# Optimization experiments

Hardware: AMD Instinct MI355X
Metric: run time of the kernel (lower is better)

## Reference

```python
import math
import jax, jax.numpy as jnp
import numpy as np

L = 2          # num_layers
B = 2          # micro batch
S = 2048       # seq_length
H = 1024       # hidden_size
NH = 16        # num_attention_heads
DH = 64        # kv_channels (head dim)
FF = 4096      # ffn_hidden_size
EPS = 1e-5
STD = 0.0048


def setup_inputs() -> dict:
    key = jax.random.key(0)
    ks = jax.random.split(key, 12)
    out_std = STD / math.sqrt(2.0 * L)
    # ALiBi slopes for NH=16 (power of 2)
    start = 2.0 ** (-2.0 ** (-(math.log2(NH) - 3)))
    slopes = np.array([start * start ** i for i in range(NH)], dtype=np.float32)
    alibi = slopes[None, :, None, None] * np.arange(S, dtype=np.float32)[None, None, None, :]
    alibi = jnp.asarray(np.broadcast_to(alibi, (B, NH, 1, S)))  # [B, NH, 1, S]
    return {
        "hidden_states": jax.random.normal(ks[0], (B, S, H), jnp.float32),
        "alibi": alibi,
        "qkv_w": jax.random.normal(ks[1], (L, 3 * NH * DH, H), jnp.float32) * STD,
        "qkv_b": jnp.zeros((L, 3 * NH * DH), jnp.float32),
        "dense_w": jax.random.normal(ks[2], (L, H, NH * DH), jnp.float32) * out_std,
        "dense_b": jnp.zeros((L, H), jnp.float32),
        "mlp_w1": jax.random.normal(ks[3], (L, FF, H), jnp.float32) * STD,
        "mlp_b1": jnp.zeros((L, FF), jnp.float32),
        "mlp_w2": jax.random.normal(ks[4], (L, H, FF), jnp.float32) * out_std,
        "mlp_b2": jnp.zeros((L, H), jnp.float32),
        "ln1_w": jnp.ones((L, H), jnp.float32),
        "ln1_b": jnp.zeros((L, H), jnp.float32),
        "ln2_w": jnp.ones((L, H), jnp.float32),
        "ln2_b": jnp.zeros((L, H), jnp.float32),
    }


def _layernorm(x, w, b):
    mu = jnp.mean(x, axis=-1, keepdims=True)
    var = jnp.mean(jnp.square(x - mu), axis=-1, keepdims=True)
    return (x - mu) * jax.lax.rsqrt(var + EPS) * w + b


def _layer(x, alibi, causal, layer_number, qkv_w, qkv_b, dense_w, dense_b,
           mlp_w1, mlp_b1, mlp_w2, mlp_b2, ln1_w, ln1_b, ln2_w, ln2_b):
    # --- attention ---
    h = _layernorm(x, ln1_w, ln1_b)
    qkv = h @ qkv_w.T + qkv_b                       # [B, S, 3*NH*DH]
    q, k, v = jnp.split(qkv, 3, axis=-1)
    q = q.reshape(B, S, NH, DH).transpose(0, 2, 1, 3)  # [B, NH, S, DH]
    k = k.reshape(B, S, NH, DH).transpose(0, 2, 1, 3)
    v = v.reshape(B, S, NH, DH).transpose(0, 2, 1, 3)
    norm_factor = math.sqrt(DH) * layer_number
    beta = 1.0 / layer_number
    alpha = 1.0 / norm_factor
    scores = beta * alibi + alpha * jnp.einsum("bhqd,bhkd->bhqk", q, k)
    # ScaleMaskSoftmax: scale by layer_number, causal mask fill -10000, softmax
    scores = scores * layer_number
    scores = jnp.where(causal, scores, jnp.float32(-10000.0))
    probs = jax.nn.softmax(scores, axis=-1)
    ctx = jnp.einsum("bhqk,bhkd->bhqd", probs, v)   # [B, NH, S, DH]
    ctx = ctx.transpose(0, 2, 1, 3).reshape(B, S, NH * DH)
    attn_out = ctx @ dense_w.T + dense_b
    x = x + attn_out
    # --- MLP ---
    h2 = _layernorm(x, ln2_w, ln2_b)
    m = jax.nn.gelu(h2 @ mlp_w1.T + mlp_b1, approximate=False)
    m = m @ mlp_w2.T + mlp_b2
    return x + m


def reference(hidden_states, alibi, qkv_w, qkv_b, dense_w, dense_b,
              mlp_w1, mlp_b1, mlp_w2, mlp_b2, ln1_w, ln1_b, ln2_w, ln2_b):
    causal = jnp.tril(jnp.ones((S, S), dtype=bool))[None, None]  # [1,1,S,S]
    x = hidden_states
    for l in range(L):
        x = _layer(x, alibi, causal, l + 1,
                   qkv_w[l], qkv_b[l], dense_w[l], dense_b[l],
                   mlp_w1[l], mlp_b1[l], mlp_w2[l], mlp_b2[l],
                   ln1_w[l], ln1_b[l], ln2_w[l], ln2_b[l])
    return x
```

## Files before the change

kernel.cpp:

```cpp
#include <hip/hip_runtime.h>
#include <cstdint>
#include <cmath>

#define SS 2048
#define HH 1024

typedef __bf16 bf16_t;
typedef __bf16 bf16x8 __attribute__((ext_vector_type(8)));
typedef __bf16 bf16x4 __attribute__((ext_vector_type(4)));
typedef float  f32x4  __attribute__((ext_vector_type(4)));

union U32P { unsigned u; bf16_t h[2]; };

__device__ __forceinline__ void async_load16(const void* g, void* l) {
  __builtin_amdgcn_global_load_lds(
      (__attribute__((address_space(1))) void*)(g),
      (__attribute__((address_space(3))) void*)(l), 16, 0, 0);
}

__global__ __launch_bounds__(256) void cvt_kernel(const float* __restrict__ in,
                                                  bf16_t* __restrict__ out) {
  size_t i = (size_t)blockIdx.x * 256 + threadIdx.x;
  f32x4 v = ((const f32x4*)in)[i];
  bf16x4 o;
  o[0] = (bf16_t)v[0]; o[1] = (bf16_t)v[1]; o[2] = (bf16_t)v[2]; o[3] = (bf16_t)v[3];
  ((bf16x4*)out)[i] = o;
}

__global__ __launch_bounds__(256) void ln_kernel(const float* __restrict__ x,
                                                 const float* __restrict__ w,
                                                 const float* __restrict__ b,
                                                 bf16_t* __restrict__ out) {
  const int row = blockIdx.x;
  const int tid = threadIdx.x;
  const f32x4 v = ((const f32x4*)(x + (size_t)row * HH))[tid];
  float s  = v[0] + v[1] + v[2] + v[3];
  float s2 = v[0]*v[0] + v[1]*v[1] + v[2]*v[2] + v[3]*v[3];
#pragma unroll
  for (int o = 1; o < 64; o <<= 1) { s += __shfl_xor(s, o); s2 += __shfl_xor(s2, o); }
  __shared__ float r1[4], r2[4];
  if ((tid & 63) == 0) { r1[tid >> 6] = s; r2[tid >> 6] = s2; }
  __syncthreads();
  float ts  = r1[0] + r1[1] + r1[2] + r1[3];
  float ts2 = r2[0] + r2[1] + r2[2] + r2[3];
  float mu  = ts * (1.0f / HH);
  float var = ts2 * (1.0f / HH) - mu * mu;
  float rstd = rsqrtf(var + 1e-5f);
  f32x4 wv = ((const f32x4*)w)[tid];
  f32x4 bv = ((const f32x4*)b)[tid];
  bf16x4 o;
#pragma unroll
  for (int j = 0; j < 4; ++j) o[j] = (bf16_t)((v[j] - mu) * rstd * wv[j] + bv[j]);
  ((bf16x4*)(out + (size_t)row * HH))[tid] = o;
}

__device__ __forceinline__ float gelu_f(float x) {
  return 0.5f * x * (1.0f + erff(x * 0.70710678118654752f));
}

__global__ __launch_bounds__(256) void fuse_add(float* __restrict__ x,
                                                const bf16_t* __restrict__ p0,
                                                const bf16_t* __restrict__ p1,
                                                const float* __restrict__ bias) {
  size_t i = (size_t)blockIdx.x * 256 + threadIdx.x;
  f32x4 xv = ((f32x4*)x)[i];
  bf16x4 a = ((const bf16x4*)p0)[i];
  bf16x4 b4 = ((const bf16x4*)p1)[i];
  f32x4 bv = ((const f32x4*)bias)[i & 255];
#pragma unroll
  for (int j = 0; j < 4; ++j) xv[j] += (float)a[j] + (float)b4[j] + bv[j];
  ((f32x4*)x)[i] = xv;
}

template <int EPI>
__global__ __launch_bounds__(256) void gemm_bt(const bf16_t* __restrict__ A,
                                               const bf16_t* __restrict__ W,
                                               const float* __restrict__ bias,
                                               bf16_t* __restrict__ outb,
                                               int M, int N, int K) {
  __shared__ __align__(16) bf16_t As[128 * 64];
  __shared__ __align__(16) bf16_t Bs[128 * 64];
  const int tid = threadIdx.x;
  const int w = tid >> 6, lane = tid & 63;
  const int m16 = lane & 15, quad = lane >> 4;
  const int wm = w & 1, wn = w >> 1;
  const int n0 = blockIdx.x * 128, m0 = blockIdx.y * 128;

  f32x4 acc[4][4];
#pragma unroll
  for (int i = 0; i < 4; ++i)
#pragma unroll
    for (int j = 0; j < 4; ++j) acc[i][j] = (f32x4){0.f, 0.f, 0.f, 0.f};

  int rowi[4], gci[4];
#pragma unroll
  for (int i = 0; i < 4; ++i) {
    int p = (w * 4 + i) * 64 + lane;
    rowi[i] = p >> 3;
    gci[i] = ((lane & 7) ^ (rowi[i] & 7)) * 8;
  }

  for (int kt = 0; kt < K; kt += 64) {
    __syncthreads();
#pragma unroll
    for (int i = 0; i < 4; ++i) {
      async_load16(A + (size_t)(m0 + rowi[i]) * K + kt + gci[i], &As[(w * 4 + i) * 512]);
      async_load16(W + (size_t)(n0 + rowi[i]) * K + kt + gci[i], &Bs[(w * 4 + i) * 512]);
    }
    __syncthreads();
#pragma unroll
    for (int kk = 0; kk < 2; ++kk) {
      bf16x8 af[4], bfv[4];
#pragma unroll
      for (int mi = 0; mi < 4; ++mi) {
        int row = wm * 64 + mi * 16 + m16;
        int cpos = (kk * 4 + quad) ^ (row & 7);
        af[mi] = *(const bf16x8*)&As[row * 64 + cpos * 8];
      }
#pragma unroll
      for (int ni = 0; ni < 4; ++ni) {
        int row = wn * 64 + ni * 16 + m16;
        int cpos = (kk * 4 + quad) ^ (row & 7);
        bfv[ni] = *(const bf16x8*)&Bs[row * 64 + cpos * 8];
      }
#pragma unroll
      for (int mi = 0; mi < 4; ++mi)
#pragma unroll
        for (int ni = 0; ni < 4; ++ni)
          acc[mi][ni] = __builtin_amdgcn_mfma_f32_16x16x32_bf16(af[mi], bfv[ni],
                                                                acc[mi][ni], 0, 0, 0);
    }
  }

#pragma unroll
  for (int ni = 0; ni < 4; ++ni) {
    int col = n0 + wn * 64 + ni * 16 + m16;
    float bv = bias[col];
#pragma unroll
    for (int mi = 0; mi < 4; ++mi) {
      int rowb = m0 + wm * 64 + mi * 16 + quad * 4;
#pragma unroll
      for (int r = 0; r < 4; ++r) {
        size_t idx = (size_t)(rowb + r) * N + col;
        float v = acc[mi][ni][r] + bv;
        if constexpr (EPI == 1) v = gelu_f(v);
        outb[idx] = (bf16_t)v;
      }
    }
  }
}

__global__ __launch_bounds__(256) void gemm_sk2(const bf16_t* __restrict__ A,
                                                const bf16_t* __restrict__ W,
                                                bf16_t* __restrict__ p0,
                                                bf16_t* __restrict__ p1,
                                                int M, int N, int K) {
  __shared__ __align__(16) bf16_t As[128 * 64];
  __shared__ __align__(16) bf16_t Bs[128 * 64];
  const int tid = threadIdx.x;
  const int w = tid >> 6, lane = tid & 63;
  const int m16 = lane & 15, quad = lane >> 4;
  const int wm = w & 1, wn = w >> 1;
  const int n0 = blockIdx.x * 128, m0 = blockIdx.y * 128;
  const int z = blockIdx.z;
  const int kbeg = z * (K >> 1), kend = kbeg + (K >> 1);
  bf16_t* outb = z ? p1 : p0;

  f32x4 acc[4][4];
#pragma unroll
  for (int i = 0; i < 4; ++i)
#pragma unroll
    for (int j = 0; j < 4; ++j) acc[i][j] = (f32x4){0.f, 0.f, 0.f, 0.f};

  int rowi[4], gci[4];
#pragma unroll
  for (int i = 0; i < 4; ++i) {
    int p = (w * 4 + i) * 64 + lane;
    rowi[i] = p >> 3;
    gci[i] = ((lane & 7) ^ (rowi[i] & 7)) * 8;
  }

  for (int kt = kbeg; kt < kend; kt += 64) {
    __syncthreads();
#pragma unroll
    for (int i = 0; i < 4; ++i) {
      async_load16(A + (size_t)(m0 + rowi[i]) * K + kt + gci[i], &As[(w * 4 + i) * 512]);
      async_load16(W + (size_t)(n0 + rowi[i]) * K + kt + gci[i], &Bs[(w * 4 + i) * 512]);
    }
    __syncthreads();
#pragma unroll
    for (int kk = 0; kk < 2; ++kk) {
      bf16x8 af[4], bfv[4];
#pragma unroll
      for (int mi = 0; mi < 4; ++mi) {
        int row = wm * 64 + mi * 16 + m16;
        int cpos = (kk * 4 + quad) ^ (row & 7);
        af[mi] = *(const bf16x8*)&As[row * 64 + cpos * 8];
      }
#pragma unroll
      for (int ni = 0; ni < 4; ++ni) {
        int row = wn * 64 + ni * 16 + m16;
        int cpos = (kk * 4 + quad) ^ (row & 7);
        bfv[ni] = *(const bf16x8*)&Bs[row * 64 + cpos * 8];
      }
#pragma unroll
      for (int mi = 0; mi < 4; ++mi)
#pragma unroll
        for (int ni = 0; ni < 4; ++ni)
          acc[mi][ni] = __builtin_amdgcn_mfma_f32_16x16x32_bf16(af[mi], bfv[ni],
                                                                acc[mi][ni], 0, 0, 0);
    }
  }

#pragma unroll
  for (int ni = 0; ni < 4; ++ni) {
    int col = n0 + wn * 64 + ni * 16 + m16;
#pragma unroll
    for (int mi = 0; mi < 4; ++mi) {
      int rowb = m0 + wm * 64 + mi * 16 + quad * 4;
#pragma unroll
      for (int r = 0; r < 4; ++r) {
        size_t idx = (size_t)(rowb + r) * N + col;
        outb[idx] = (bf16_t)acc[mi][ni][r];
      }
    }
  }
}

__global__ __launch_bounds__(256) void attn_kernel(const bf16_t* __restrict__ qkv,
                                                   bf16_t* __restrict__ ctx) {
  const int qt = 31 - blockIdx.y;
  const int bh = blockIdx.x;
  const int b = bh >> 4, h = bh & 15;
  const int tid = threadIdx.x;
  const int w = tid >> 6, lane = tid & 63;
  const int m16 = lane & 15, quad = lane >> 4;

  __shared__ __align__(16) bf16_t Vt[2][64 * 72];
  __shared__ __align__(16) bf16_t Pl[4][16 * 72];

  const float slope2 = __builtin_amdgcn_exp2f(-0.70710678118654752f * (float)(h + 1))
                       * 1.4426950408889634f;
  const int wt = (int)((30.0f / slope2 + 63.0f) * 0.015625f);
  const int kt0 = (qt - wt > 0) ? (qt - wt) : 0;

  const int q_abs = qt * 64 + w * 16 + m16;
  float alkb[16];
#pragma unroll
  for (int kn = 0; kn < 4; ++kn)
#pragma unroll
    for (int r = 0; r < 4; ++r)
      alkb[kn * 4 + r] = slope2 * (float)(kt0 * 64 + kn * 16 + quad * 4 + r - q_abs);
  const float d64 = slope2 * 64.0f;

  const int qrow = qt * 64 + w * 16 + m16;
  const bf16_t* qbase = qkv + (size_t)(b * SS + qrow) * 3072 + h * 64;
  const bf16x8 bq0 = *(const bf16x8*)(qbase + quad * 8);
  const bf16x8 bq1 = *(const bf16x8*)(qbase + 32 + quad * 8);

  const bf16_t* kbase = qkv + (size_t)(b * SS + m16) * 3072 + 1024 + h * 64 + quad * 8;
  const int kp2 = (tid & 31) * 2, vd0 = (tid >> 5) * 8;
  const bf16_t* vsrc = qkv + (size_t)(b * SS + kp2) * 3072 + 2048 + h * 64 + vd0;
  const int ql = w * 16 + m16;
  constexpr float C = 0.18033688011112042f;

  f32x4 acc[4];
#pragma unroll
  for (int i = 0; i < 4; ++i) acc[i] = (f32x4){0.f, 0.f, 0.f, 0.f};
  float rs_l = 0.f;

  bf16x8 ak[4][2], v0, v1;
  {
    const bf16_t* kb = kbase + (size_t)kt0 * 64 * 3072;
#pragma unroll
    for (int kn = 0; kn < 4; ++kn) {
      ak[kn][0] = *(const bf16x8*)(kb + (size_t)(kn * 16) * 3072);
      ak[kn][1] = *(const bf16x8*)(kb + (size_t)(kn * 16) * 3072 + 32);
    }
    const bf16_t* vs = vsrc + (size_t)kt0 * 64 * 3072;
    v0 = *(const bf16x8*)(vs);
    v1 = *(const bf16x8*)(vs + 3072);
  }
#pragma unroll
  for (int j = 0; j < 8; ++j) {
    U32P pk; pk.h[0] = v0[j]; pk.h[1] = v1[j];
    *(unsigned*)&Vt[kt0 & 1][(vd0 + j) * 72 + kp2] = pk.u;
  }

  for (int kt = kt0; kt <= qt; ++kt) {
    __syncthreads();

    bf16x8 nk[4][2], nv0 = v0, nv1 = v1;
    if (kt < qt) {
      const bf16_t* kb = kbase + (size_t)(kt + 1) * 64 * 3072;
#pragma unroll
      for (int kn = 0; kn < 4; ++kn) {
        nk[kn][0] = *(const bf16x8*)(kb + (size_t)(kn * 16) * 3072);
        nk[kn][1] = *(const bf16x8*)(kb + (size_t)(kn * 16) * 3072 + 32);
      }
      const bf16_t* nsrc = vsrc + (size_t)(kt + 1) * 64 * 3072;
      nv0 = *(const bf16x8*)(nsrc);
      nv1 = *(const bf16x8*)(nsrc + 3072);
    } else {
#pragma unroll
      for (int kn = 0; kn < 4; ++kn) { nk[kn][0] = ak[kn][0]; nk[kn][1] = ak[kn][1]; }
    }

    float p[16];
    const bool diag = (kt == qt);
#pragma unroll
    for (int kn = 0; kn < 4; ++kn) {
      f32x4 z = (f32x4){0.f, 0.f, 0.f, 0.f};
      z = __builtin_amdgcn_mfma_f32_16x16x32_bf16(ak[kn][0], bq0, z, 0, 0, 0);
      z = __builtin_amdgcn_mfma_f32_16x16x32_bf16(ak[kn][1], bq1, z, 0, 0, 0);
#pragma unroll
      for (int r = 0; r < 4; ++r) {
        float s = fmaf(z[r], C, alkb[kn * 4 + r]);
        if (diag) {
          int kl = kn * 16 + quad * 4 + r;
          if (kl > ql) s = -INFINITY;
        }
        float e = __builtin_amdgcn_exp2f(s);
        p[kn * 4 + r] = e;
        rs_l += e;
      }
    }
#pragma unroll
    for (int i = 0; i < 16; ++i) alkb[i] += d64;

#pragma unroll
    for (int kn = 0; kn < 4; ++kn) {
      U32P a, c;
      a.h[0] = (bf16_t)p[kn * 4 + 0]; a.h[1] = (bf16_t)p[kn * 4 + 1];
      c.h[0] = (bf16_t)p[kn * 4 + 2]; c.h[1] = (bf16_t)p[kn * 4 + 3];
      uint2 pk; pk.x = a.u; pk.y = c.u;
      *(uint2*)&Pl[w][m16 * 72 + kn * 16 + quad * 4] = pk;
    }
    const bf16_t* vt = &Vt[kt & 1][0];
    bf16x8 bp0 = *(const bf16x8*)&Pl[w][m16 * 72 + quad * 8];
    bf16x8 bp1 = *(const bf16x8*)&Pl[w][m16 * 72 + 32 + quad * 8];
#pragma unroll
    for (int ni = 0; ni < 4; ++ni) {
      bf16x8 av0 = *(const bf16x8*)&vt[(ni * 16 + m16) * 72 + quad * 8];
      bf16x8 av1 = *(const bf16x8*)&vt[(ni * 16 + m16) * 72 + 32 + quad * 8];
      acc[ni] = __builtin_amdgcn_mfma_f32_16x16x32_bf16(av0, bp0, acc[ni], 0, 0, 0);
      acc[ni] = __builtin_amdgcn_mfma_f32_16x16x32_bf16(av1, bp1, acc[ni], 0, 0, 0);
    }

    if (kt < qt) {
#pragma unroll
      for (int j = 0; j < 8; ++j) {
        U32P pk; pk.h[0] = nv0[j]; pk.h[1] = nv1[j];
        *(unsigned*)&Vt[(kt + 1) & 1][(vd0 + j) * 72 + kp2] = pk.u;
      }
    }
#pragma unroll
    for (int kn = 0; kn < 4; ++kn) { ak[kn][0] = nk[kn][0]; ak[kn][1] = nk[kn][1]; }
    v0 = nv0; v1 = nv1;
  }

  rs_l += __shfl_xor(rs_l, 16);
  rs_l += __shfl_xor(rs_l, 32);
  const float inv_l = 1.0f / rs_l;
  bf16_t* cb = ctx + (size_t)(b * SS + qt * 64 + w * 16 + m16) * 1024 + h * 64;
#pragma unroll
  for (int ni = 0; ni < 4; ++ni) {
    U32P a, c;
    a.h[0] = (bf16_t)(acc[ni][0] * inv_l); a.h[1] = (bf16_t)(acc[ni][1] * inv_l);
    c.h[0] = (bf16_t)(acc[ni][2] * inv_l); c.h[1] = (bf16_t)(acc[ni][3] * inv_l);
    uint2 pk; pk.x = a.u; pk.y = c.u;
    *(uint2*)(cb + ni * 16 + quad * 4) = pk;
  }
}

extern "C" void kernel_launch(void* const* d_in, const int* in_sizes, int n_in,
                              void* d_out, int out_size, void* d_ws, size_t ws_size,
                              hipStream_t stream) {
  const float* hs    = (const float*)d_in[0];
  const float* qkvw  = (const float*)d_in[2];
  const float* qkvb  = (const float*)d_in[3];
  const float* dw    = (const float*)d_in[4];
  const float* db    = (const float*)d_in[5];
  const float* w1    = (const float*)d_in[6];
  const float* b1    = (const float*)d_in[7];
  const float* w2    = (const float*)d_in[8];
  const float* b2    = (const float*)d_in[9];
  const float* ln1w  = (const float*)d_in[10];
  const float* ln1b  = (const float*)d_in[11];
  const float* ln2w  = (const float*)d_in[12];
  const float* ln2b  = (const float*)d_in[13];
  float* x = (float*)d_out;

  char* ws = (char*)d_ws;
  bf16_t* wqc = (bf16_t*)(ws + 0);
  bf16_t* wdc = (bf16_t*)(ws + 12582912);
  bf16_t* w1c = (bf16_t*)(ws + 16777216);
  bf16_t* w2c = (bf16_t*)(ws + 33554432);
  bf16_t* hb  = (bf16_t*)(ws + 50331648);
  bf16_t* qm  = (bf16_t*)(ws + 58720256);
  bf16_t* cx  = (bf16_t*)(ws + 92274688);
  bf16_t* dp0 = qm;
  bf16_t* dp1 = qm + (size_t)4096 * 1024;

  hipMemcpyAsync(x, hs, (size_t)4096 * 1024 * 4, hipMemcpyDeviceToDevice, stream);
  cvt_kernel<<<6144, 256, 0, stream>>>(qkvw, wqc);
  cvt_kernel<<<2048, 256, 0, stream>>>(dw, wdc);
  cvt_kernel<<<8192, 256, 0, stream>>>(w1, w1c);
  cvt_kernel<<<8192, 256, 0, stream>>>(w2, w2c);

  for (int l = 0; l < 2; ++l) {
    ln_kernel<<<4096, 256, 0, stream>>>(x, ln1w + l * 1024, ln1b + l * 1024, hb);
    gemm_bt<0><<<dim3(24, 32), 256, 0, stream>>>(hb, wqc + (size_t)l * 3145728,
        qkvb + l * 3072, qm, 4096, 3072, 1024);
    attn_kernel<<<dim3(32, 32), 256, 0, stream>>>(qm, cx);
    gemm_sk2<<<dim3(8, 32, 2), 256, 0, stream>>>(cx, wdc + (size_t)l * 1048576,
        dp0, dp1, 4096, 1024, 1024);
    fuse_add<<<4096, 256, 0, stream>>>(x, dp0, dp1, db + l * 1024);
    ln_kernel<<<4096, 256, 0, stream>>>(x, ln2w + l * 1024, ln2b + l * 1024, hb);
    gemm_bt<1><<<dim3(32, 32), 256, 0, stream>>>(hb, w1c + (size_t)l * 4194304,
        b1 + l * 4096, qm, 4096, 4096, 1024);
    gemm_sk2<<<dim3(8, 32, 2), 256, 0, stream>>>(qm, w2c + (size_t)l * 4194304,
        hb, cx, 4096, 1024, 4096);
    fuse_add<<<4096, 256, 0, stream>>>(x, hb, cx, b2 + l * 1024);
  }
}
```

Before: 705.7 us.

## Double-buffer GEMM shared-memory tiles and fuse residual add with layernorm

Both bf16 GEMM kernels now keep two LDS tiles per operand. The next K-tile is prefetched with async global-to-LDS loads while the current one is fed to MFMA, which cuts the two barriers per iteration down to one and overlaps load latency with compute. Separately, the residual add of the split-K partial sums is fused with the following layernorm in a new fuse_add_ln kernel, so x is not re-read in a separate LN pass. The doubled LDS footprint (64 KB per block) may lower the number of blocks resident per CU.

```diff
diff --git a/kernel.cpp b/kernel.cpp
--- a/kernel.cpp
+++ b/kernel.cpp
@@ -72,14 +72,51 @@
   ((f32x4*)x)[i] = xv;
 }
 
+__global__ __launch_bounds__(256) void fuse_add_ln(float* __restrict__ x,
+                                                   const bf16_t* __restrict__ p0,
+                                                   const bf16_t* __restrict__ p1,
+                                                   const float* __restrict__ bias,
+                                                   const float* __restrict__ lw,
+                                                   const float* __restrict__ lb,
+                                                   bf16_t* __restrict__ out) {
+  const int row = blockIdx.x;
+  const int tid = threadIdx.x;
+  const size_t i = (size_t)row * 256 + tid;
+  f32x4 xv = ((f32x4*)x)[i];
+  bf16x4 a = ((const bf16x4*)p0)[i];
+  bf16x4 b4 = ((const bf16x4*)p1)[i];
+  f32x4 bv = ((const f32x4*)bias)[tid];
+#pragma unroll
+  for (int j = 0; j < 4; ++j) xv[j] += (float)a[j] + (float)b4[j] + bv[j];
+  ((f32x4*)x)[i] = xv;
+  float s  = xv[0] + xv[1] + xv[2] + xv[3];
+  float s2 = xv[0]*xv[0] + xv[1]*xv[1] + xv[2]*xv[2] + xv[3]*xv[3];
+#pragma unroll
+  for (int o = 1; o < 64; o <<= 1) { s += __shfl_xor(s, o); s2 += __shfl_xor(s2, o); }
+  __shared__ float r1[4], r2[4];
+  if ((tid & 63) == 0) { r1[tid >> 6] = s; r2[tid >> 6] = s2; }
+  __syncthreads();
+  float ts  = r1[0] + r1[1] + r1[2] + r1[3];
+  float ts2 = r2[0] + r2[1] + r2[2] + r2[3];
+  float mu  = ts * (1.0f / HH);
+  float var = ts2 * (1.0f / HH) - mu * mu;
+  float rstd = rsqrtf(var + 1e-5f);
+  f32x4 wv  = ((const f32x4*)lw)[tid];
+  f32x4 lbv = ((const f32x4*)lb)[tid];
+  bf16x4 o;
+#pragma unroll
+  for (int j = 0; j < 4; ++j) o[j] = (bf16_t)((xv[j] - mu) * rstd * wv[j] + lbv[j]);
+  ((bf16x4*)(out + (size_t)row * HH))[tid] = o;
+}
+
 template <int EPI>
 __global__ __launch_bounds__(256) void gemm_bt(const bf16_t* __restrict__ A,
                                                const bf16_t* __restrict__ W,
                                                const float* __restrict__ bias,
                                                bf16_t* __restrict__ outb,
                                                int M, int N, int K) {
-  __shared__ __align__(16) bf16_t As[128 * 64];
-  __shared__ __align__(16) bf16_t Bs[128 * 64];
+  __shared__ __align__(16) bf16_t As[2][128 * 64];
+  __shared__ __align__(16) bf16_t Bs[2][128 * 64];
   const int tid = threadIdx.x;
   const int w = tid >> 6, lane = tid & 63;
   const int m16 = lane & 15, quad = lane >> 4;
@@ -100,14 +137,26 @@
     gci[i] = ((lane & 7) ^ (rowi[i] & 7)) * 8;
   }
 
-  for (int kt = 0; kt < K; kt += 64) {
+#pragma unroll
+  for (int i = 0; i < 4; ++i) {
+    async_load16(A + (size_t)(m0 + rowi[i]) * K + gci[i], &As[0][(w * 4 + i) * 512]);
+    async_load16(W + (size_t)(n0 + rowi[i]) * K + gci[i], &Bs[0][(w * 4 + i) * 512]);
+  }
+
+  const int NT = K >> 6;
+  for (int t = 0; t < NT; ++t) {
+    const int cur = t & 1;
     __syncthreads();
-#pragma unroll
-    for (int i = 0; i < 4; ++i) {
-      async_load16(A + (size_t)(m0 + rowi[i]) * K + kt + gci[i], &As[(w * 4 + i) * 512]);
-      async_load16(W + (size_t)(n0 + rowi[i]) * K + kt + gci[i], &Bs[(w * 4 + i) * 512]);
-    }
-    __syncthreads();
+    if (t + 1 < NT) {
+      const int kt = (t + 1) << 6;
+#pragma unroll
+      for (int i = 0; i < 4; ++i) {
+        async_load16(A + (size_t)(m0 + rowi[i]) * K + kt + gci[i],
+                     &As[cur ^ 1][(w * 4 + i) * 512]);
+        async_load16(W + (size_t)(n0 + rowi[i]) * K + kt + gci[i],
+                     &Bs[cur ^ 1][(w * 4 + i) * 512]);
+      }
+    }
 #pragma unroll
     for (int kk = 0; kk < 2; ++kk) {
       bf16x8 af[4], bfv[4];
@@ -115,13 +164,13 @@
       for (int mi = 0; mi < 4; ++mi) {
         int row = wm * 64 + mi * 16 + m16;
         int cpos = (kk * 4 + quad) ^ (row & 7);
-        af[mi] = *(const bf16x8*)&As[row * 64 + cpos * 8];
+        af[mi] = *(const bf16x8*)&As[cur][row * 64 + cpos * 8];
       }
 #pragma unroll
       for (int ni = 0; ni < 4; ++ni) {
         int row = wn * 64 + ni * 16 + m16;
         int cpos = (kk * 4 + quad) ^ (row & 7);
-        bfv[ni] = *(const bf16x8*)&Bs[row * 64 + cpos * 8];
+        bfv[ni] = *(const bf16x8*)&Bs[cur][row * 64 + cpos * 8];
       }
 #pragma unroll
       for (int mi = 0; mi < 4; ++mi)
@@ -155,15 +204,15 @@
                                                 bf16_t* __restrict__ p0,
                                                 bf16_t* __restrict__ p1,
                                                 int M, int N, int K) {
-  __shared__ __align__(16) bf16_t As[128 * 64];
-  __shared__ __align__(16) bf16_t Bs[128 * 64];
+  __shared__ __align__(16) bf16_t As[2][128 * 64];
+  __shared__ __align__(16) bf16_t Bs[2][128 * 64];
   const int tid = threadIdx.x;
   const int w = tid >> 6, lane = tid & 63;
   const int m16 = lane & 15, quad = lane >> 4;
   const int wm = w & 1, wn = w >> 1;
   const int n0 = blockIdx.x * 128, m0 = blockIdx.y * 128;
   const int z = blockIdx.z;
-  const int kbeg = z * (K >> 1), kend = kbeg + (K >> 1);
+  const int kbeg = z * (K >> 1);
   bf16_t* outb = z ? p1 : p0;
 
   f32x4 acc[4][4];
@@ -180,14 +229,26 @@
     gci[i] = ((lane & 7) ^ (rowi[i] & 7)) * 8;
   }
 
-  for (int kt = kbeg; kt < kend; kt += 64) {
+#pragma unroll
+  for (int i = 0; i < 4; ++i) {
+    async_load16(A + (size_t)(m0 + rowi[i]) * K + kbeg + gci[i], &As[0][(w * 4 + i) * 512]);
+    async_load16(W + (size_t)(n0 + rowi[i]) * K + kbeg + gci[i], &Bs[0][(w * 4 + i) * 512]);
+  }
+
+  const int NT = K >> 7;
+  for (int t = 0; t < NT; ++t) {
+    const int cur = t & 1;
     __syncthreads();
-#pragma unroll
-    for (int i = 0; i < 4; ++i) {
-      async_load16(A + (size_t)(m0 + rowi[i]) * K + kt + gci[i], &As[(w * 4 + i) * 512]);
-      async_load16(W + (size_t)(n0 + rowi[i]) * K + kt + gci[i], &Bs[(w * 4 + i) * 512]);
-    }
-    __syncthreads();
+    if (t + 1 < NT) {
+      const int kt = kbeg + ((t + 1) << 6);
+#pragma unroll
+      for (int i = 0; i < 4; ++i) {
+        async_load16(A + (size_t)(m0 + rowi[i]) * K + kt + gci[i],
+                     &As[cur ^ 1][(w * 4 + i) * 512]);
+        async_load16(W + (size_t)(n0 + rowi[i]) * K + kt + gci[i],
+                     &Bs[cur ^ 1][(w * 4 + i) * 512]);
+      }
+    }
 #pragma unroll
     for (int kk = 0; kk < 2; ++kk) {
       bf16x8 af[4], bfv[4];
@@ -195,13 +256,13 @@
       for (int mi = 0; mi < 4; ++mi) {
         int row = wm * 64 + mi * 16 + m16;
         int cpos = (kk * 4 + quad) ^ (row & 7);
-        af[mi] = *(const bf16x8*)&As[row * 64 + cpos * 8];
+        af[mi] = *(const bf16x8*)&As[cur][row * 64 + cpos * 8];
       }
 #pragma unroll
       for (int ni = 0; ni < 4; ++ni) {
         int row = wn * 64 + ni * 16 + m16;
         int cpos = (kk * 4 + quad) ^ (row & 7);
-        bfv[ni] = *(const bf16x8*)&Bs[row * 64 + cpos * 8];
+        bfv[ni] = *(const bf16x8*)&Bs[cur][row * 64 + cpos * 8];
       }
 #pragma unroll
       for (int mi = 0; mi < 4; ++mi)
@@ -408,19 +469,25 @@
   cvt_kernel<<<8192, 256, 0, stream>>>(w1, w1c);
   cvt_kernel<<<8192, 256, 0, stream>>>(w2, w2c);
 
+  ln_kernel<<<4096, 256, 0, stream>>>(x, ln1w, ln1b, hb);
+
   for (int l = 0; l < 2; ++l) {
-    ln_kernel<<<4096, 256, 0, stream>>>(x, ln1w + l * 1024, ln1b + l * 1024, hb);
     gemm_bt<0><<<dim3(24, 32), 256, 0, stream>>>(hb, wqc + (size_t)l * 3145728,
         qkvb + l * 3072, qm, 4096, 3072, 1024);
     attn_kernel<<<dim3(32, 32), 256, 0, stream>>>(qm, cx);
     gemm_sk2<<<dim3(8, 32, 2), 256, 0, stream>>>(cx, wdc + (size_t)l * 1048576,
         dp0, dp1, 4096, 1024, 1024);
-    fuse_add<<<4096, 256, 0, stream>>>(x, dp0, dp1, db + l * 1024);
-    ln_kernel<<<4096, 256, 0, stream>>>(x, ln2w + l * 1024, ln2b + l * 1024, hb);
+    fuse_add_ln<<<4096, 256, 0, stream>>>(x, dp0, dp1, db + l * 1024,
+        ln2w + l * 1024, ln2b + l * 1024, hb);
     gemm_bt<1><<<dim3(32, 32), 256, 0, stream>>>(hb, w1c + (size_t)l * 4194304,
         b1 + l * 4096, qm, 4096, 4096, 1024);
     gemm_sk2<<<dim3(8, 32, 2), 256, 0, stream>>>(qm, w2c + (size_t)l * 4194304,
         hb, cx, 4096, 1024, 4096);
-    fuse_add<<<4096, 256, 0, stream>>>(x, hb, cx, b2 + l * 1024);
-  }
-}
+    if (l == 0) {
+      fuse_add_ln<<<4096, 256, 0, stream>>>(x, hb, cx, b2,
+          ln1w + 1024, ln1b + 1024, hb);
+    } else {
+      fuse_add<<<4096, 256, 0, stream>>>(x, hb, cx, b2 + 1024);
+    }
+  }
+}
```

New measurement: 674.8 us. 1.05x faster.
